# Kernel tuning notes

Hardware: AMD Instinct MI355X
Metric: run time of the kernel (lower is better)

## Reference

```python
import jax, jax.numpy as jnp
import numpy as np

B, N, H, E, OBS, A, AFF, EFF = 2, 50000, 64, 1_000_000, 128, 18, 512, 256


def setup_inputs() -> dict:
    key = jax.random.key(0)
    ks = jax.random.split(key, 20)
    s = 0.05  # small init to keep gates/tanh unsaturated
    return {
        "obs": jax.random.normal(ks[0], (B, OBS), jnp.float32),
        "state": jax.random.normal(ks[1], (B, N, H), jnp.float32) * 0.1,
        "W_in": jax.random.normal(ks[2], (OBS, H), jnp.float32) * s,
        "b_in": jnp.zeros((H,), jnp.float32),
        "W_msg": jax.random.normal(ks[3], (H, H), jnp.float32) * s,
        "W_gate": jax.random.normal(ks[4], (2 * H, H), jnp.float32) * s,
        "b_gate": jnp.zeros((H,), jnp.float32),
        "W_cand": jax.random.normal(ks[5], (2 * H, H), jnp.float32) * s,
        "b_cand": jnp.zeros((H,), jnp.float32),
        "W_dec": jax.random.normal(ks[6], (H, H), jnp.float32) * s,
        "b_dec": jnp.zeros((H,), jnp.float32),
        "W_mean": jax.random.normal(ks[7], (H, A), jnp.float32) * s,
        "b_mean": jnp.zeros((A,), jnp.float32),
        "W_ls": jax.random.normal(ks[8], (H, A), jnp.float32) * s,
        "b_ls": jnp.zeros((A,), jnp.float32),
        "src_index": jax.random.randint(ks[9], (E,), 0, N),
        "dst_index": jax.random.randint(ks[10], (E,), 0, N),
        "afferent_idx": jax.random.randint(ks[11], (AFF,), 0, N),
        "efferent_idx": jax.random.randint(ks[12], (EFF,), 0, N),
    }


def reference(obs, state, W_in, b_in, W_msg, W_gate, b_gate, W_cand, b_cand,
              W_dec, b_dec, W_mean, b_mean, W_ls, b_ls,
              src_index, dst_index, afferent_idx, efferent_idx):
    # inject obs projection into afferent node slots
    projected = obs @ W_in + b_in                                   # [B, H]
    injected = jnp.zeros_like(state).at[:, afferent_idx, :].set(projected[:, None, :])
    # gather-project-scatter message passing over the edge list
    src_msgs = state[:, src_index, :] @ W_msg                       # [B, E, H]
    messages = jnp.zeros_like(state).at[:, dst_index, :].add(src_msgs)
    # GRU-style gated update
    combined = messages + injected
    gate_in = jnp.concatenate([state, combined], axis=-1)           # [B, N, 2H]
    z = jax.nn.sigmoid(gate_in @ W_gate + b_gate)
    cand = jnp.tanh(gate_in @ W_cand + b_cand)
    next_state = (1.0 - z) * state + z * cand
    # mean-pool readout over efferent nodes, then policy heads
    readout = next_state[:, efferent_idx, :].mean(axis=1)           # [B, H]
    decoded = jnp.tanh(readout @ W_dec + b_dec)
    mean = decoded @ W_mean + b_mean
    log_std = jnp.clip(decoded @ W_ls + b_ls, -5.0, 2.0)
    return mean, log_std, next_state
```

## Files before the change

kernel.cpp:

```cpp
#include <hip/hip_runtime.h>
#include <hip/hip_bf16.h>

constexpr int kN   = 50000;
constexpr int kH   = 64;
constexpr int kB   = 2;
constexpr int kE   = 1000000;
constexpr int kObs = 128;
constexpr int kA   = 18;
constexpr int kAff = 512;
constexpr int kEff = 256;
constexpr int kNH  = kN * kH;
constexpr int kOutOff = 2 * kB * kA;
constexpr int kRanges = 8;
constexpr int kNr  = kN / kRanges;
constexpr int kChunks = 64;
constexpr int kEc  = kE / kChunks;
constexpr int kHistB = kRanges * kChunks;
constexpr int kPackBlocks = (kNH + 8191) / 8192;
constexpr int kWprepBlocks = 20;
constexpr int kScanB = (kN + 255) / 256;
constexpr int kGatB = kRanges * 1563;
constexpr int kUpdB = (kN + 31) / 32;

typedef __attribute__((ext_vector_type(8))) short short8_t;
typedef __attribute__((ext_vector_type(4))) float f32x4_t;

__device__ __forceinline__ float ldf(const void* p, int i, int f32) {
  if (f32) return ((const float*)p)[i];
  unsigned short u = ((const unsigned short*)p)[i];
  union { unsigned int x; float f; } v; v.x = ((unsigned int)u) << 16; return v.f;
}
__device__ __forceinline__ void stf(void* p, int i, float val, int f32) {
  if (f32) ((float*)p)[i] = val;
  else ((__hip_bfloat16*)p)[i] = __float2bfloat16(val);
}
__device__ __forceinline__ float lo16(unsigned int w) {
  union { unsigned int i; float f; } v; v.i = w << 16; return v.f;
}
__device__ __forceinline__ float hi16(unsigned int w) {
  union { unsigned int i; float f; } v; v.i = w & 0xffff0000u; return v.f;
}
__device__ __forceinline__ float b2f(unsigned short u) {
  union { unsigned int i; float f; } v; v.i = ((unsigned int)u) << 16; return v.f;
}
__device__ __forceinline__ unsigned int f2b(float f) {
  union { float f; unsigned int u; } v; v.f = f;
  unsigned int r = v.u + 0x7fffu + ((v.u >> 16) & 1u);
  return r >> 16;
}
__device__ __forceinline__ float fsig(float x) {
  return __builtin_amdgcn_rcpf(1.f + __expf(-x));
}
__device__ __forceinline__ float ftanh(float x) {
  return 1.f - 2.f * __builtin_amdgcn_rcpf(__expf(2.f * x) + 1.f);
}
__device__ __forceinline__ int detect64(const unsigned short* wprobe, int t) {
  int hits = 0;
  for (int k = 0; k < 4; ++k) {
    unsigned short u = wprobe[(t * 4 + k) * 2];
    int e = (u >> 7) & 0xFF;
    if ((u & 0x7FFFu) != 0 && e >= 108 && e <= 128) hits++;
  }
  for (int off = 32; off; off >>= 1) hits += __shfl_down(hits, off);
  return (hits < 128) ? 1 : 0;
}

extern "C" __global__ __launch_bounds__(1024) void k_prep(
    const unsigned short* __restrict__ wprobe,
    const void* __restrict__ obs,
    const void* __restrict__ W_in,
    const void* __restrict__ b_in,
    const int* __restrict__ aff_idx,
    const int* __restrict__ dst,
    const void* __restrict__ W_msg,
    const void* __restrict__ W_gate,
    const void* __restrict__ W_cand,
    int* __restrict__ dflag,
    int* __restrict__ flags,
    float* __restrict__ projected,
    int* __restrict__ deg_c,
    unsigned short* __restrict__ wt,
    float* __restrict__ eff_acc) {
  __shared__ int sdeg[kNr];
  int t = threadIdx.x, b = blockIdx.x;
  if (b == 0) {
    __shared__ int sflag;
    if (t < 64) { int f = detect64(wprobe, t); if (t == 0) { sflag = f; dflag[0] = f; } }
    for (int i = t; i < kN; i += 1024) flags[i] = 0;
    if (t < 128) eff_acc[t] = 0.f;
    __syncthreads();
    int f32 = sflag;
    if (t < kAff) flags[aff_idx[t]] = 1;
    if (t < kB * kH) {
      int bb = t >> 6, h = t & 63;
      float acc = ldf(b_in, h, f32);
      for (int o = 0; o < kObs; ++o)
        acc += ldf(obs, bb * kObs + o, f32) * ldf(W_in, o * kH + h, f32);
      projected[t] = acc;
    }
  } else if (b <= kHistB) {
    int h = b - 1, r = h & 7, c = h >> 3;
    int r0 = r * kNr;
    for (int i = t; i < kNr; i += 1024) sdeg[i] = 0;
    __syncthreads();
    int end = (c + 1) * kEc;
    for (int e = c * kEc + t; e < end; e += 1024) {
      unsigned rel = (unsigned)(dst[e] - r0);
      if (rel < (unsigned)kNr) atomicAdd(&sdeg[rel], 1);
    }
    __syncthreads();
    for (int i = t; i < kNr; i += 1024) deg_c[c * kN + r0 + i] = sdeg[i];
  } else {
    __shared__ int sflag;
    if (t < 64) { int f = detect64(wprobe, t); if (t == 0) sflag = f; }
    __syncthreads();
    int f32 = sflag;
    int i = (b - 1 - kHistB) * 1024 + t;
    if (i < 4096) {
      int n = i >> 6, k = i & 63;
      wt[i] = (unsigned short)f2b(ldf(W_msg, k * 64 + n, f32));
    } else if (i < 12288) {
      int j = i - 4096; int n = j >> 7, k = j & 127;
      wt[i] = (unsigned short)f2b(ldf(W_gate, k * 64 + n, f32));
    } else if (i < 20480) {
      int j = i - 12288; int n = j >> 7, k = j & 127;
      wt[i] = (unsigned short)f2b(ldf(W_cand, k * 64 + n, f32));
    }
  }
}

extern "C" __global__ void k_scan1(const int* __restrict__ deg_c,
                                   int* __restrict__ row_off,
                                   int* __restrict__ partials) {
  __shared__ int sd[256];
  int t = threadIdx.x;
  int n = blockIdx.x * 256 + t;
  int s = 0;
  if (n < kN) {
    for (int c = 0; c < kChunks; ++c) s += deg_c[c * kN + n];
  }
  sd[t] = s;
  __syncthreads();
  for (int off = 1; off < 256; off <<= 1) {
    int v = (t >= off) ? sd[t - off] : 0;
    __syncthreads();
    sd[t] += v;
    __syncthreads();
  }
  int excl = sd[t] - s;
  if (t == 255) partials[blockIdx.x] = sd[255];
  if (n < kN) row_off[n] = excl;
}

extern "C" __global__ void k_scan3(int* __restrict__ row_off,
                                   const int* __restrict__ partials,
                                   int* __restrict__ deg_c) {
  __shared__ int sd[256];
  int t = threadIdx.x;
  int s = 0;
  for (int j = t; j < (int)blockIdx.x; j += 256) s += partials[j];
  sd[t] = s;
  __syncthreads();
  for (int off = 128; off; off >>= 1) {
    if (t < off) sd[t] += sd[t + off];
    __syncthreads();
  }
  int base = sd[0];
  int n = blockIdx.x * 256 + t;
  if (n < kN) {
    int v = row_off[n] + base;
    row_off[n] = v;
    int run = v;
#pragma unroll 8
    for (int c = 0; c < kChunks; ++c) {
      int d = deg_c[c * kN + n];
      deg_c[c * kN + n] = run;
      run += d;
    }
  }
  if (blockIdx.x == 0 && t == 0) row_off[kN] = kE;
}

extern "C" __global__ __launch_bounds__(1024) void k_scatter(
    const int* __restrict__ src,
    const int* __restrict__ dst,
    const int* __restrict__ chunk_base,
    int* __restrict__ sorted_src,
    const unsigned short* __restrict__ wprobe,
    const void* __restrict__ state,
    unsigned int* __restrict__ pack) {
  __shared__ int scur[kNr];
  int t = threadIdx.x;
  if (blockIdx.x < kHistB) {
    int r = blockIdx.x & 7, c = blockIdx.x >> 3;
    int r0 = r * kNr;
    for (int i = t; i < kNr; i += 1024) scur[i] = chunk_base[c * kN + r0 + i];
    __syncthreads();
    int end = (c + 1) * kEc;
    for (int e = c * kEc + t; e < end; e += 1024) {
      unsigned rel = (unsigned)(dst[e] - r0);
      if (rel < (unsigned)kNr) {
        int pos = atomicAdd(&scur[rel], 1);
        sorted_src[pos] = src[e];
      }
    }
  } else {
    __shared__ int sflag;
    if (t < 64) { int f = detect64(wprobe, t); if (t == 0) sflag = f; }
    __syncthreads();
    int f32 = sflag;
    int i = (blockIdx.x - kHistB) * 8192 + t * 8;
    if (i < kNH) {
      uint4 o0, o1;
      if (!f32) {
        uint4 a = *(const uint4*)((const unsigned short*)state + i);
        uint4 c4 = *(const uint4*)((const unsigned short*)state + kNH + i);
        o0.x = (a.x & 0xffffu) | (c4.x << 16);
        o0.y = (a.x >> 16)     | (c4.x & 0xffff0000u);
        o0.z = (a.y & 0xffffu) | (c4.y << 16);
        o0.w = (a.y >> 16)     | (c4.y & 0xffff0000u);
        o1.x = (a.z & 0xffffu) | (c4.z << 16);
        o1.y = (a.z >> 16)     | (c4.z & 0xffff0000u);
        o1.z = (a.w & 0xffffu) | (c4.w << 16);
        o1.w = (a.w >> 16)     | (c4.w & 0xffff0000u);
      } else {
        const float* sf = (const float*)state;
        unsigned int w[8];
#pragma unroll
        for (int k = 0; k < 8; ++k)
          w[k] = f2b(sf[i + k]) | (f2b(sf[kNH + i + k]) << 16);
        o0 = make_uint4(w[0], w[1], w[2], w[3]);
        o1 = make_uint4(w[4], w[5], w[6], w[7]);
      }
      *(uint4*)&pack[i] = o0;
      *(uint4*)&pack[i + 4] = o1;
    }
  }
}

extern "C" __global__ __launch_bounds__(256) void k_gather(
    const unsigned int* __restrict__ pack,
    const int* __restrict__ row_off,
    const int* __restrict__ sorted_src,
    unsigned int* __restrict__ agg) {
  int wave = threadIdx.x >> 6, lane = threadIdx.x & 63;
  int x = blockIdx.x & 7, j = blockIdx.x >> 3;
  int local = j * 4 + wave;
  if (local >= kNr) return;
  int n = x * kNr + local;
  int s  = row_off[n];
  int en = row_off[n + 1];
  int g = lane >> 4, col = lane & 15;
  const uint4* pk4 = (const uint4*)pack;
  float a0x = 0.f, a0y = 0.f, a0z = 0.f, a0w = 0.f;
  float a1x = 0.f, a1y = 0.f, a1z = 0.f, a1w = 0.f;
  for (int e = s; e < en; e += 8) {
#pragma unroll
    for (int h = 0; h < 2; ++h) {
      int ee = e + h * 4 + g;
      int idx = sorted_src[min(ee, en - 1)];
      uint4 wv = pk4[idx * 16 + col];
      if (ee >= en) { wv.x = 0u; wv.y = 0u; wv.z = 0u; wv.w = 0u; }
      a0x += lo16(wv.x); a1x += hi16(wv.x);
      a0y += lo16(wv.y); a1y += hi16(wv.y);
      a0z += lo16(wv.z); a1z += hi16(wv.z);
      a0w += lo16(wv.w); a1w += hi16(wv.w);
    }
  }
  a0x += __shfl_xor(a0x, 16); a0x += __shfl_xor(a0x, 32);
  a0y += __shfl_xor(a0y, 16); a0y += __shfl_xor(a0y, 32);
  a0z += __shfl_xor(a0z, 16); a0z += __shfl_xor(a0z, 32);
  a0w += __shfl_xor(a0w, 16); a0w += __shfl_xor(a0w, 32);
  a1x += __shfl_xor(a1x, 16); a1x += __shfl_xor(a1x, 32);
  a1y += __shfl_xor(a1y, 16); a1y += __shfl_xor(a1y, 32);
  a1z += __shfl_xor(a1z, 16); a1z += __shfl_xor(a1z, 32);
  a1w += __shfl_xor(a1w, 16); a1w += __shfl_xor(a1w, 32);
  if (g == 0) {
    uint4 o;
    o.x = f2b(a0x) | (f2b(a1x) << 16);
    o.y = f2b(a0y) | (f2b(a1y) << 16);
    o.z = f2b(a0z) | (f2b(a1z) << 16);
    o.w = f2b(a0w) | (f2b(a1w) << 16);
    ((uint4*)agg)[n * 16 + col] = o;
  }
}

extern "C" __global__ __launch_bounds__(256) void k_update(
    const unsigned int* __restrict__ pk,
    const unsigned short* __restrict__ wt,
    const void* __restrict__ b_gate,
    const void* __restrict__ b_cand,
    const unsigned int* __restrict__ agg,
    const int* __restrict__ flags,
    const float* __restrict__ projected,
    const int* __restrict__ dflag,
    void* __restrict__ out,
    const int* __restrict__ eff_idx,
    float* __restrict__ eff_acc) {
  __shared__ uint4 lx4[1088];
  __shared__ int smatch[256];
  __shared__ int smcnt;
  unsigned short* lx = (unsigned short*)lx4;
  int f32 = dflag[0];
  int t = threadIdx.x;
  int w = t >> 6, lane = t & 63;
  int q = lane >> 4, l15 = lane & 15;
  int rowb = w * 16;
  int nd0 = blockIdx.x * 32;
  int ndw = nd0 + w * 8;
  if (t == 0) smcnt = 0;

  const uint4* pk4 = (const uint4*)pk;
  const uint4* ag4 = (const uint4*)agg;
  for (int j = lane; j < 128; j += 64) {
    int ndl = j >> 4, c4 = j & 15;
    int ndg = min(ndw + ndl, kN - 1);
    uint4 pv = pk4[ndg * 16 + c4];
    uint4 av = ag4[ndg * 16 + c4];
    int r0 = rowb + 2 * ndl;
    *(uint2*)&lx[r0 * 136 + c4 * 4] =
        make_uint2((pv.x & 0xffffu) | (pv.y << 16), (pv.z & 0xffffu) | (pv.w << 16));
    *(uint2*)&lx[(r0 + 1) * 136 + c4 * 4] =
        make_uint2((pv.x >> 16) | (pv.y & 0xffff0000u), (pv.z >> 16) | (pv.w & 0xffff0000u));
    *(uint2*)&lx[r0 * 136 + 64 + c4 * 4] =
        make_uint2((av.x & 0xffffu) | (av.y << 16), (av.z & 0xffffu) | (av.w << 16));
    *(uint2*)&lx[(r0 + 1) * 136 + 64 + c4 * 4] =
        make_uint2((av.x >> 16) | (av.y & 0xffff0000u), (av.z >> 16) | (av.w & 0xffff0000u));
  }

  const unsigned short* wm = wt;
  const unsigned short* wg = wt + 4096;
  const unsigned short* wc = wt + 12288;

  short8_t a0 = *(const short8_t*)&lx[(rowb + l15) * 136 + 64 + q * 8];
  short8_t a1 = *(const short8_t*)&lx[(rowb + l15) * 136 + 96 + q * 8];
  f32x4_t msgc[4];
#pragma unroll
  for (int ct = 0; ct < 4; ++ct) {
    f32x4_t acc = {0.f, 0.f, 0.f, 0.f};
    short8_t b0 = *(const short8_t*)&wm[(ct * 16 + l15) * 64 + q * 8];
    short8_t b1 = *(const short8_t*)&wm[(ct * 16 + l15) * 64 + 32 + q * 8];
    acc = __builtin_amdgcn_mfma_f32_16x16x32_bf16(a0, b0, acc, 0, 0, 0);
    acc = __builtin_amdgcn_mfma_f32_16x16x32_bf16(a1, b1, acc, 0, 0, 0);
    msgc[ct] = acc;
  }
  int nA = ndw + q * 2, nB = nA + 1;
  int flA = (nA < kN) ? flags[nA] : 0;
  int flB = (nB < kN) ? flags[nB] : 0;
#pragma unroll
  for (int ct = 0; ct < 4; ++ct) {
    int col = ct * 16 + l15;
    float pj0 = projected[col], pj1 = projected[64 + col];
#pragma unroll
    for (int r = 0; r < 4; ++r) {
      int row = rowb + q * 4 + r;
      int fl = (r < 2) ? flA : flB;
      float inj = fl ? ((row & 1) ? pj1 : pj0) : 0.f;
      lx[row * 136 + 64 + col] = (unsigned short)f2b(msgc[ct][r] + inj);
    }
  }

  short8_t xa[4];
#pragma unroll
  for (int ks = 0; ks < 4; ++ks)
    xa[ks] = *(const short8_t*)&lx[(rowb + l15) * 136 + ks * 32 + q * 8];
  float ps[16];
#pragma unroll
  for (int ct = 0; ct < 4; ++ct)
#pragma unroll
    for (int rp = 0; rp < 2; ++rp) {
      int row = rowb + q * 4 + 2 * rp;
      ps[ct * 4 + rp * 2 + 0] = b2f(lx[row * 136 + ct * 16 + l15]);
      ps[ct * 4 + rp * 2 + 1] = b2f(lx[(row + 1) * 136 + ct * 16 + l15]);
    }
  float* soutw = (float*)((char*)lx4 + w * 4352);
#pragma unroll
  for (int ct = 0; ct < 4; ++ct) {
    f32x4_t accg = {0.f, 0.f, 0.f, 0.f}, accc = {0.f, 0.f, 0.f, 0.f};
#pragma unroll
    for (int ks = 0; ks < 4; ++ks) {
      short8_t bg = *(const short8_t*)&wg[(ct * 16 + l15) * 128 + ks * 32 + q * 8];
      short8_t bc = *(const short8_t*)&wc[(ct * 16 + l15) * 128 + ks * 32 + q * 8];
      accg = __builtin_amdgcn_mfma_f32_16x16x32_bf16(xa[ks], bg, accg, 0, 0, 0);
      accc = __builtin_amdgcn_mfma_f32_16x16x32_bf16(xa[ks], bc, accc, 0, 0, 0);
    }
    int col = ct * 16 + l15;
    float bgv = ldf(b_gate, col, f32), bcv = ldf(b_cand, col, f32);
#pragma unroll
    for (int rp = 0; rp < 2; ++rp) {
      int r = q * 4 + 2 * rp;
      float z0 = fsig(accg[2 * rp] + bgv);
      float c0 = ftanh(accc[2 * rp] + bcv);
      soutw[r * 64 + col] = (1.f - z0) * ps[ct * 4 + rp * 2 + 0] + z0 * c0;
      float z1 = fsig(accg[2 * rp + 1] + bgv);
      float c1 = ftanh(accc[2 * rp + 1] + bcv);
      soutw[(r + 1) * 64 + col] = (1.f - z1) * ps[ct * 4 + rp * 2 + 1] + z1 * c1;
    }
  }
  __syncthreads();

  if (t < kEff) {
    unsigned rel = (unsigned)(eff_idx[t] - nd0);
    if (rel < 32u) { int s = atomicAdd(&smcnt, 1); smatch[s] = (int)rel; }
  }
  __syncthreads();

  int nvalid = min(32, kN - nd0) * 64;
  if (f32) {
    float* po = (float*)out + kOutOff;
#pragma unroll
    for (int p = 0; p < 2; ++p)
      for (int j = t * 4; j < nvalid; j += 1024) {
        int ndl = j >> 6, c = j & 63;
        int wv = ndl >> 3, r = ((ndl & 7) << 1) + p;
        float4 v = *(float4*)((char*)lx4 + wv * 4352 + r * 256 + c * 4);
        *(float4*)(po + p * kNH + nd0 * 64 + j) = v;
      }
  } else {
    unsigned short* po = (unsigned short*)out + kOutOff;
#pragma unroll
    for (int p = 0; p < 2; ++p)
      for (int j = t * 8; j < nvalid; j += 2048) {
        int ndl = j >> 6, c = j & 63;
        int wv = ndl >> 3, r = ((ndl & 7) << 1) + p;
        const char* base = (const char*)lx4 + wv * 4352 + r * 256 + c * 4;
        float4 v0 = *(const float4*)base;
        float4 v1 = *(const float4*)(base + 16);
        uint4 o;
        o.x = f2b(v0.x) | (f2b(v0.y) << 16);
        o.y = f2b(v0.z) | (f2b(v0.w) << 16);
        o.z = f2b(v1.x) | (f2b(v1.y) << 16);
        o.w = f2b(v1.z) | (f2b(v1.w) << 16);
        *(uint4*)(po + p * kNH + nd0 * 64 + j) = o;
      }
  }

  int cnt = smcnt;
  for (int m = 0; m < cnt; ++m) {
    int rel = smatch[m];
    if (t < 128) {
      int p = t >> 6, c = t & 63;
      int wv = rel >> 3, r = ((rel & 7) << 1) + p;
      float v = *(const float*)((const char*)lx4 + wv * 4352 + r * 256 + c * 4);
      if (!f32) v = b2f((unsigned short)f2b(v));
      atomicAdd(&eff_acc[p * 64 + c], v);
    }
  }
}

extern "C" __global__ void k_readout(const void* __restrict__ W_dec,
                                     const void* __restrict__ b_dec,
                                     const void* __restrict__ W_mean,
                                     const void* __restrict__ b_mean,
                                     const void* __restrict__ W_ls,
                                     const void* __restrict__ b_ls,
                                     const float* __restrict__ eff_acc,
                                     const int* __restrict__ dflag,
                                     void* __restrict__ out) {
  __shared__ float ro[128], dec[128];
  int f32 = dflag[0];
  int t = threadIdx.x;
  if (t < 128) ro[t] = eff_acc[t] * (1.f / kEff);
  __syncthreads();
  if (t < 128) {
    int bb = t >> 6, h = t & 63;
    float d = ldf(b_dec, h, f32);
    for (int k = 0; k < 64; ++k) d += ro[bb * 64 + k] * ldf(W_dec, k * 64 + h, f32);
    dec[t] = tanhf(d);
  }
  __syncthreads();
  if (t < kB * kA) {
    int bb = t / kA, a = t % kA;
    float m = ldf(b_mean, a, f32), l = ldf(b_ls, a, f32);
    for (int k = 0; k < 64; ++k) {
      float dv = dec[bb * 64 + k];
      m += dv * ldf(W_mean, k * kA + a, f32);
      l += dv * ldf(W_ls, k * kA + a, f32);
    }
    l = fminf(fmaxf(l, -5.f), 2.f);
    stf(out, t, m, f32);
    stf(out, kB * kA + t, l, f32);
  }
}

extern "C" void kernel_launch(void* const* d_in, const int* in_sizes, int n_in,
                              void* d_out, int out_size, void* d_ws, size_t ws_size,
                              hipStream_t stream) {
  (void)in_sizes; (void)n_in; (void)out_size; (void)ws_size;
  const void* obs    = d_in[0];
  const void* state  = d_in[1];
  const void* W_in   = d_in[2];
  const void* b_in   = d_in[3];
  const void* W_msg  = d_in[4];
  const void* W_gate = d_in[5];
  const void* b_gate = d_in[6];
  const void* W_cand = d_in[7];
  const void* b_cand = d_in[8];
  const void* W_dec  = d_in[9];
  const void* b_dec  = d_in[10];
  const void* W_mean = d_in[11];
  const void* b_mean = d_in[12];
  const void* W_ls   = d_in[13];
  const void* b_ls   = d_in[14];
  const int* src = (const int*)d_in[15];
  const int* dst = (const int*)d_in[16];
  const int* aff = (const int*)d_in[17];
  const int* eff = (const int*)d_in[18];

  int* wsp        = (int*)d_ws;
  int* flags      = wsp;
  int* deg_c      = flags + kN;
  int* row_off    = deg_c + kChunks * kN;
  int* partials   = row_off + (kN + 64);
  int* dflag      = partials + 512;
  float* projected = (float*)(dflag + 16);
  float* eff_acc   = projected + 128;
  int* sorted_src  = (int*)(eff_acc + 128);
  unsigned int* pk  = (unsigned int*)(sorted_src + kE);
  unsigned int* agg = pk + kNH;
  unsigned short* wt = (unsigned short*)(agg + kNH);

  k_prep<<<1 + kHistB + kWprepBlocks, 1024, 0, stream>>>(
      (const unsigned short*)W_cand, obs, W_in, b_in, aff, dst,
      W_msg, W_gate, W_cand, dflag, flags, projected, deg_c, wt, eff_acc);
  k_scan1<<<kScanB, 256, 0, stream>>>(deg_c, row_off, partials);
  k_scan3<<<kScanB, 256, 0, stream>>>(row_off, partials, deg_c);
  k_scatter<<<kHistB + kPackBlocks, 1024, 0, stream>>>(
      src, dst, deg_c, sorted_src, (const unsigned short*)W_cand, state, pk);
  k_gather<<<kGatB, 256, 0, stream>>>(pk, row_off, sorted_src, agg);
  k_update<<<kUpdB, 256, 0, stream>>>(pk, wt, b_gate, b_cand,
                                      agg, flags, projected, dflag, d_out,
                                      eff, eff_acc);
  k_readout<<<1, 128, 0, stream>>>(W_dec, b_dec, W_mean, b_mean, W_ls, b_ls,
                                   eff_acc, dflag, d_out);
}
```

Before: 260.0 us.

## Interleave pack and update block indices across node ranges

Remaps block indices in the state-pack and GRU update kernels so consecutive blocks cycle through the eight node ranges (range = blockIdx & 7), with per-range bounds instead of a global tail check. This likely matches how the gather stage is partitioned by range, so each range's data becomes ready or is consumed in an order that spreads memory traffic and aligns with per-range work (e.g. XCD/L2 locality on a chiplet GPU). It adds early-exit blocks when a range's block count is rounded up, plus a little index arithmetic.

```diff
diff --git a/kernel.cpp b/kernel.cpp
--- a/kernel.cpp
+++ b/kernel.cpp
@@ -16,11 +16,13 @@
 constexpr int kChunks = 64;
 constexpr int kEc  = kE / kChunks;
 constexpr int kHistB = kRanges * kChunks;
-constexpr int kPackBlocks = (kNH + 8191) / 8192;
+constexpr int kPackPerR = (kNr + 127) / 128;
+constexpr int kPackBlocks = kRanges * kPackPerR;
 constexpr int kWprepBlocks = 20;
 constexpr int kScanB = (kN + 255) / 256;
 constexpr int kGatB = kRanges * 1563;
-constexpr int kUpdB = (kN + 31) / 32;
+constexpr int kUpdPerR = (kNr + 31) / 32;
+constexpr int kUpdB = kRanges * kUpdPerR;
 
 typedef __attribute__((ext_vector_type(8))) short short8_t;
 typedef __attribute__((ext_vector_type(4))) float f32x4_t;
@@ -209,8 +211,12 @@
     if (t < 64) { int f = detect64(wprobe, t); if (t == 0) sflag = f; }
     __syncthreads();
     int f32 = sflag;
-    int i = (blockIdx.x - kHistB) * 8192 + t * 8;
-    if (i < kNH) {
+    int p = blockIdx.x - kHistB;
+    int x = p & 7, j = p >> 3;
+    int nb = x * kNr + j * 128;
+    int nl = min(nb + 128, (x + 1) * kNr);
+    int i = nb * 64 + t * 8;
+    if (i < nl * 64) {
       uint4 o0, o1;
       if (!f32) {
         uint4 a = *(const uint4*)((const unsigned short*)state + i);
@@ -306,7 +312,10 @@
   int w = t >> 6, lane = t & 63;
   int q = lane >> 4, l15 = lane & 15;
   int rowb = w * 16;
-  int nd0 = blockIdx.x * 32;
+  int x = blockIdx.x & 7, jb = blockIdx.x >> 3;
+  int nd0 = x * kNr + jb * 32;
+  int rend = (x + 1) * kNr;
+  if (nd0 >= rend) return;
   int ndw = nd0 + w * 8;
   if (t == 0) smcnt = 0;
 
@@ -314,7 +323,7 @@
   const uint4* ag4 = (const uint4*)agg;
   for (int j = lane; j < 128; j += 64) {
     int ndl = j >> 4, c4 = j & 15;
-    int ndg = min(ndw + ndl, kN - 1);
+    int ndg = min(ndw + ndl, rend - 1);
     uint4 pv = pk4[ndg * 16 + c4];
     uint4 av = ag4[ndg * 16 + c4];
     int r0 = rowb + 2 * ndl;
@@ -345,8 +354,8 @@
     msgc[ct] = acc;
   }
   int nA = ndw + q * 2, nB = nA + 1;
-  int flA = (nA < kN) ? flags[nA] : 0;
-  int flB = (nB < kN) ? flags[nB] : 0;
+  int flA = (nA < rend) ? flags[nA] : 0;
+  int flB = (nB < rend) ? flags[nB] : 0;
 #pragma unroll
   for (int ct = 0; ct < 4; ++ct) {
     int col = ct * 16 + l15;
@@ -399,13 +408,14 @@
   }
   __syncthreads();
 
+  int nlim = min(32, rend - nd0);
   if (t < kEff) {
     unsigned rel = (unsigned)(eff_idx[t] - nd0);
-    if (rel < 32u) { int s = atomicAdd(&smcnt, 1); smatch[s] = (int)rel; }
+    if (rel < (unsigned)nlim) { int s = atomicAdd(&smcnt, 1); smatch[s] = (int)rel; }
   }
   __syncthreads();
 
-  int nvalid = min(32, kN - nd0) * 64;
+  int nvalid = nlim * 64;
   if (f32) {
     float* po = (float*)out + kOutOff;
 #pragma unroll
```

After: 257.4 us. About the same (-1.0%).
